# Kernel optimization log

Hardware: AMD Instinct MI355X
Metric: run time of the kernel (lower is better)

Reference implementation:

```python
import jax, jax.numpy as jnp
import numpy as np

N_NODES = 50000
N_EDGES = 400000
D_IN = 2048
D_OUT = 512


def setup_inputs() -> dict:
    key = jax.random.key(0)
    k1, k2, k3 = jax.random.split(key, 3)
    x = jax.random.normal(k1, (N_NODES, D_IN), dtype=jnp.float32)
    edge_index = jax.random.randint(k2, (2, N_EDGES), 0, N_NODES, dtype=jnp.int64)
    # Glorot init like PyG GCNConv
    scale = jnp.sqrt(6.0 / (D_IN + D_OUT)).astype(jnp.float32)
    weight = jax.random.uniform(k3, (D_IN, D_OUT), dtype=jnp.float32, minval=-scale, maxval=scale)
    bias = jnp.zeros((D_OUT,), dtype=jnp.float32)
    return {"x": x, "edge_index": edge_index, "weight": weight, "bias": bias}


def reference(x, edge_index, weight, bias):
    N = x.shape[0]
    # GCNConv(normalize=True): add self-loops, symmetric deg^-1/2 normalization
    loops = jnp.arange(N, dtype=edge_index.dtype)
    src = jnp.concatenate([edge_index[0], loops])  # message sources (x_j)
    dst = jnp.concatenate([edge_index[1], loops])  # aggregation targets
    ones = jnp.ones(dst.shape[0], dtype=x.dtype)
    deg = jax.ops.segment_sum(ones, dst, num_segments=N)  # [N]
    deg_inv_sqrt = jnp.where(deg > 0, jax.lax.rsqrt(deg), 0.0)
    norm = deg_inv_sqrt[src] * deg_inv_sqrt[dst]  # [E+N]
    h = x @ weight  # [N, d_out] linear transform before propagation
    msgs = norm[:, None] * h[src]  # [E+N, d_out]
    out = jax.ops.segment_sum(msgs, dst, num_segments=N) + bias  # [N, d_out]
    return jax.nn.log_softmax(out, axis=1)
```

## Files before the change

kernel.cpp:

```cpp
#include <hip/hip_runtime.h>
#include <stdint.h>

#define D_IN   2048
#define D_OUT  512

typedef __bf16 bf16;
typedef bf16     bf16x8 __attribute__((ext_vector_type(8)));
typedef float    f32x4  __attribute__((ext_vector_type(4)));
typedef uint32_t u32x4  __attribute__((ext_vector_type(4)));

#define GLP(p)  (const __attribute__((address_space(1))) void*)(p)
#define LDSP(p) (__attribute__((address_space(3))) void*)(p)

__global__ void k_count(const int* __restrict__ dstv, int* __restrict__ cnt, int E) {
    int e = blockIdx.x * blockDim.x + threadIdx.x;
    if (e < E) atomicAdd(&cnt[dstv[e]], 1);
}

__global__ void k_dis(const int* __restrict__ cnt, float* __restrict__ dis, int n) {
    int i = blockIdx.x * blockDim.x + threadIdx.x;
    if (i < n) dis[i] = rsqrtf((float)(cnt[i] + 1));
}

__global__ __launch_bounds__(1024) void k_scan1(const int* __restrict__ cnt,
                                                int* __restrict__ offs,
                                                int* __restrict__ bsum, int n) {
    __shared__ int wsum[16], wbase[16];
    const int tid = threadIdx.x, lane = tid & 63, wv = tid >> 6;
    int i = blockIdx.x * 1024 + tid;
    int v = (i < n) ? cnt[i] : 0;
    int x = v;
    #pragma unroll
    for (int d = 1; d < 64; d <<= 1) {
        int y = __shfl_up(x, d);
        if (lane >= d) x += y;
    }
    if (lane == 63) wsum[wv] = x;
    __syncthreads();
    if (tid < 16) {
        int s = 0;
        for (int j = 0; j < tid; ++j) s += wsum[j];
        wbase[tid] = s;
    }
    __syncthreads();
    if (i < n) offs[i] = wbase[wv] + x - v;
    if (tid == 0) bsum[blockIdx.x] = wbase[15] + wsum[15];
}

__global__ void k_scan2(int* __restrict__ bsum, int nb) {
    int t = threadIdx.x;
    if (nb <= 64) {
        int v = (t < nb) ? bsum[t] : 0;
        int x = v;
        #pragma unroll
        for (int d = 1; d < 64; d <<= 1) {
            int y = __shfl_up(x, d);
            if (t >= d) x += y;
        }
        if (t < nb) bsum[t] = x - v;
    } else if (t == 0) {
        int run = 0;
        for (int j = 0; j < nb; ++j) { int v = bsum[j]; bsum[j] = run; run += v; }
    }
}

__global__ void k_scan3(int* __restrict__ offs, const int* __restrict__ bsum, int n) {
    int i = blockIdx.x * blockDim.x + threadIdx.x;
    if (i < n) offs[i] += bsum[i >> 10];
}

__global__ void k_fill(const int* __restrict__ srcv, const int* __restrict__ dstv,
                       const int* __restrict__ offs, int* __restrict__ cur,
                       int* __restrict__ csr, int E) {
    int e = blockIdx.x * blockDim.x + threadIdx.x;
    if (e < E) {
        int d = dstv[e];
        int p = offs[d] + atomicAdd(&cur[d], 1);
        csr[p] = srcv[e];
    }
}

__global__ void k_wt(const float* __restrict__ W, uint16_t* __restrict__ wt) {
    __shared__ float t[32][33];
    int kb = blockIdx.x * 32, nb = blockIdx.y * 32;
    int tx = threadIdx.x, ty = threadIdx.y;
    #pragma unroll
    for (int i = 0; i < 32; i += 8)
        t[ty + i][tx] = W[(size_t)(kb + ty + i) * D_OUT + nb + tx];
    __syncthreads();
    bf16* o = (bf16*)wt;
    #pragma unroll
    for (int i = 0; i < 32; i += 8)
        o[(size_t)(nb + ty + i) * D_IN + kb + tx] = (bf16)t[tx][ty + i];
}

__global__ __launch_bounds__(256) void k_gemm(const float* __restrict__ X,
                                              const uint16_t* __restrict__ WT,
                                              uint16_t* __restrict__ H, int M) {
    __shared__ float    lsA[2][128 * 32];
    __shared__ uint16_t lsB[128 * 64];
    const int nwg = gridDim.x;
    const int b = blockIdx.x;
    const int q = nwg >> 3, r = nwg & 7;
    const int xcd = b & 7, lo = b >> 3;
    const int g = (xcd < r) ? (xcd * (q + 1) + lo) : (r * (q + 1) + (xcd - r) * q + lo);
    const int m0 = (g >> 2) * 128;
    const int n0 = (g & 3) * 128;
    const int tid = threadIdx.x;
    const int w = tid >> 6, lane = tid & 63;
    const int wr = w >> 1, wc = w & 1;
    const int lr = lane & 15, lk = lane >> 4;

    f32x4 acc[4][4];
    #pragma unroll
    for (int m = 0; m < 4; m++)
        #pragma unroll
        for (int n = 0; n < 4; n++) acc[m][n] = (f32x4)(0.0f);

    const float* aSrc[2][4];
    const uint16_t* bSrc[4];
    #pragma unroll
    for (int j = 0; j < 4; j++) {
        int c = w * 4 + j;
        int uidx = c * 64 + lane;
        int row = uidx >> 3, u = uidx & 7;
        int lrow = row;
        if (m0 + row >= M) lrow = (M - 1) - m0;
        const float* rbase = X + (size_t)(m0 + lrow) * D_IN;
        #pragma unroll
        for (int h = 0; h < 2; h++)
            aSrc[h][j] = rbase + h * 32 + (u ^ (row & 7)) * 4;
        bSrc[j] = WT + (size_t)(n0 + row) * D_IN + (u ^ (row & 7)) * 8;
    }

    for (int k0 = 0; k0 < D_IN; k0 += 64) {
        #pragma unroll
        for (int h = 0; h < 2; h++)
            #pragma unroll
            for (int j = 0; j < 4; j++)
                __builtin_amdgcn_global_load_lds(GLP(aSrc[h][j] + k0),
                                                 LDSP(lsA[h] + (w * 4 + j) * 256), 16, 0, 0);
        #pragma unroll
        for (int j = 0; j < 4; j++)
            __builtin_amdgcn_global_load_lds(GLP(bSrc[j] + k0),
                                             LDSP(lsB + (w * 4 + j) * 512), 16, 0, 0);
        __syncthreads();

        #pragma unroll
        for (int kk = 0; kk < 2; kk++) {
            bf16x8 aF[4], bF[4];
            #pragma unroll
            for (int m = 0; m < 4; m++) {
                int row = wr * 64 + m * 16 + lr;
                const float* base = lsA[kk] + row * 32;
                f32x4 a0 = *(const f32x4*)(base + (((2 * lk)    ) ^ (row & 7)) * 4);
                f32x4 a1 = *(const f32x4*)(base + (((2 * lk) + 1) ^ (row & 7)) * 4);
                bf16x8 af;
                af[0] = (bf16)a0[0]; af[1] = (bf16)a0[1]; af[2] = (bf16)a0[2]; af[3] = (bf16)a0[3];
                af[4] = (bf16)a1[0]; af[5] = (bf16)a1[1]; af[6] = (bf16)a1[2]; af[7] = (bf16)a1[3];
                aF[m] = af;
            }
            #pragma unroll
            for (int n = 0; n < 4; n++) {
                int row = wc * 64 + n * 16 + lr;
                bF[n] = *(const bf16x8*)((const bf16*)lsB + row * 64 + (((kk * 4 + lk) ^ (row & 7)) * 8));
            }
            #pragma unroll
            for (int m = 0; m < 4; m++)
                #pragma unroll
                for (int n = 0; n < 4; n++)
                    acc[m][n] = __builtin_amdgcn_mfma_f32_16x16x32_bf16(aF[m], bF[n], acc[m][n], 0, 0, 0);
        }
        __syncthreads();
    }

    #pragma unroll
    for (int m = 0; m < 4; m++) {
        int rbase = m0 + wr * 64 + m * 16 + lk * 4;
        #pragma unroll
        for (int n = 0; n < 4; n++) {
            int col = n0 + wc * 64 + n * 16 + lr;
            #pragma unroll
            for (int j = 0; j < 4; j++) {
                int row = rbase + j;
                if (row < M) {
                    bf16 t = (bf16)acc[m][n][j];
                    H[(size_t)row * D_OUT + col] = __builtin_bit_cast(uint16_t, t);
                }
            }
        }
    }
}

__global__ __launch_bounds__(256) void k_agg(const uint16_t* __restrict__ h,
                                             const int* __restrict__ csr,
                                             const int* __restrict__ offs,
                                             const int* __restrict__ cnt,
                                             const float* __restrict__ dis,
                                             const float* __restrict__ bias,
                                             float* __restrict__ out, int N) {
    const int wv = threadIdx.x >> 6, lane = threadIdx.x & 63;
    const int i = blockIdx.x * 4 + wv;
    if (i >= N) return;
    const float di = dis[i];
    float acc[8];
    {
        u32x4 v = *(const u32x4*)(h + (size_t)i * D_OUT + lane * 8);
        float s2 = di * di;
        #pragma unroll
        for (int k = 0; k < 4; k++) {
            acc[2 * k]     = __builtin_bit_cast(float, v[k] << 16) * s2;
            acc[2 * k + 1] = __builtin_bit_cast(float, v[k] & 0xffff0000u) * s2;
        }
    }
    const int o = offs[i], c = cnt[i];
    for (int e = o; e < o + c; ++e) {
        int s = csr[e];
        float ws = di * dis[s];
        u32x4 v = *(const u32x4*)(h + (size_t)s * D_OUT + lane * 8);
        #pragma unroll
        for (int k = 0; k < 4; k++) {
            acc[2 * k]     += __builtin_bit_cast(float, v[k] << 16) * ws;
            acc[2 * k + 1] += __builtin_bit_cast(float, v[k] & 0xffff0000u) * ws;
        }
    }
    {
        const f32x4* bp = (const f32x4*)(bias + lane * 8);
        f32x4 b0 = bp[0], b1 = bp[1];
        #pragma unroll
        for (int k = 0; k < 4; k++) { acc[k] += b0[k]; acc[4 + k] += b1[k]; }
    }
    float mx = acc[0];
    #pragma unroll
    for (int k = 1; k < 8; k++) mx = fmaxf(mx, acc[k]);
    #pragma unroll
    for (int d = 1; d < 64; d <<= 1) mx = fmaxf(mx, __shfl_xor(mx, d));
    float se = 0.f;
    #pragma unroll
    for (int k = 0; k < 8; k++) se += expf(acc[k] - mx);
    #pragma unroll
    for (int d = 1; d < 64; d <<= 1) se += __shfl_xor(se, d);
    float lse = mx + logf(se);
    f32x4 o0, o1;
    #pragma unroll
    for (int k = 0; k < 4; k++) { o0[k] = acc[k] - lse; o1[k] = acc[4 + k] - lse; }
    f32x4* op = (f32x4*)(out + (size_t)i * D_OUT + lane * 8);
    op[0] = o0; op[1] = o1;
}

extern "C" void kernel_launch(void* const* d_in, const int* in_sizes, int n_in,
                              void* d_out, int out_size, void* d_ws, size_t ws_size,
                              hipStream_t stream) {
    const float* x    = (const float*)d_in[0];
    const int*   ei   = (const int*)d_in[1];
    const float* W    = (const float*)d_in[2];
    const float* bias = (const float*)d_in[3];
    float* out = (float*)d_out;

    const int N = in_sizes[0] / D_IN;
    const int E = in_sizes[1] / 2;
    const int* srcv = ei;
    const int* dstv = ei + E;

    char* p = (char*)d_ws;
    auto carve = [&](size_t b) { void* r = (void*)p; p += (b + 255) & ~(size_t)255; return r; };
    uint16_t* h    = (uint16_t*)carve((size_t)N * D_OUT * 2);
    uint16_t* wt   = (uint16_t*)carve((size_t)D_OUT * D_IN * 2);
    int*      cnt  = (int*)carve((size_t)N * 4);
    int*      cur  = (int*)carve((size_t)N * 4);
    float*    dis  = (float*)carve((size_t)N * 4);
    int*      offs = (int*)carve((size_t)N * 4);
    int*      csr  = (int*)carve((size_t)E * 4);
    int*      bsum = (int*)carve(1024 * 4);

    hipMemsetAsync(cnt, 0, ((size_t)N * 4 + 255 & ~(size_t)255) + (size_t)N * 4, stream);

    k_wt<<<dim3(D_IN / 32, D_OUT / 32), dim3(32, 8), 0, stream>>>(W, wt);
    k_count<<<(E + 255) / 256, 256, 0, stream>>>(dstv, cnt, E);
    k_dis<<<(N + 255) / 256, 256, 0, stream>>>(cnt, dis, N);
    const int nb = (N + 1023) / 1024;
    k_scan1<<<nb, 1024, 0, stream>>>(cnt, offs, bsum, N);
    k_scan2<<<1, 64, 0, stream>>>(bsum, nb);
    k_scan3<<<(N + 255) / 256, 256, 0, stream>>>(offs, bsum, N);
    k_fill<<<(E + 255) / 256, 256, 0, stream>>>(srcv, dstv, offs, cur, csr, E);

    k_gemm<<<((N + 127) / 128) * 4, 256, 0, stream>>>(x, wt, h, N);

    k_agg<<<(N + 3) / 4, 256, 0, stream>>>(h, csr, offs, cnt, dis, bias, out, N);
}
```

Baseline: 342.6 us.

## Fuse small graph-prep kernels and convert GEMM A operand to bf16 at LDS store

Folds the degree-normalization and cursor-reset work into the first scan kernel, and removes the scan-fixup kernel by adding block sums at use sites in fill and aggregate. The memset shrinks accordingly. In the GEMM, the fp32 X tile is now loaded through registers, converted to bf16 once, and stored to a swizzled bf16 LDS tile. This replaces the direct global-to-LDS fp32 copy followed by per-fragment conversion, halving LDS footprint and removing repeated converts. The cost is losing the async global_load_lds path for A, which adds register pressure and load latency inside the loop.

```diff
diff --git a/kernel.cpp b/kernel.cpp
--- a/kernel.cpp
+++ b/kernel.cpp
@@ -17,14 +17,11 @@
     if (e < E) atomicAdd(&cnt[dstv[e]], 1);
 }
 
-__global__ void k_dis(const int* __restrict__ cnt, float* __restrict__ dis, int n) {
-    int i = blockIdx.x * blockDim.x + threadIdx.x;
-    if (i < n) dis[i] = rsqrtf((float)(cnt[i] + 1));
-}
-
 __global__ __launch_bounds__(1024) void k_scan1(const int* __restrict__ cnt,
                                                 int* __restrict__ offs,
-                                                int* __restrict__ bsum, int n) {
+                                                int* __restrict__ bsum,
+                                                float* __restrict__ dis,
+                                                int* __restrict__ cur, int n) {
     __shared__ int wsum[16], wbase[16];
     const int tid = threadIdx.x, lane = tid & 63, wv = tid >> 6;
     int i = blockIdx.x * 1024 + tid;
@@ -43,7 +40,11 @@
         wbase[tid] = s;
     }
     __syncthreads();
-    if (i < n) offs[i] = wbase[wv] + x - v;
+    if (i < n) {
+        offs[i] = wbase[wv] + x - v;
+        dis[i]  = rsqrtf((float)(v + 1));
+        cur[i]  = 0;
+    }
     if (tid == 0) bsum[blockIdx.x] = wbase[15] + wsum[15];
 }
 
@@ -64,18 +65,13 @@
     }
 }
 
-__global__ void k_scan3(int* __restrict__ offs, const int* __restrict__ bsum, int n) {
-    int i = blockIdx.x * blockDim.x + threadIdx.x;
-    if (i < n) offs[i] += bsum[i >> 10];
-}
-
 __global__ void k_fill(const int* __restrict__ srcv, const int* __restrict__ dstv,
-                       const int* __restrict__ offs, int* __restrict__ cur,
-                       int* __restrict__ csr, int E) {
+                       const int* __restrict__ offs, const int* __restrict__ bsum,
+                       int* __restrict__ cur, int* __restrict__ csr, int E) {
     int e = blockIdx.x * blockDim.x + threadIdx.x;
     if (e < E) {
         int d = dstv[e];
-        int p = offs[d] + atomicAdd(&cur[d], 1);
+        int p = offs[d] + bsum[d >> 10] + atomicAdd(&cur[d], 1);
         csr[p] = srcv[e];
     }
 }
@@ -97,7 +93,7 @@
 __global__ __launch_bounds__(256) void k_gemm(const float* __restrict__ X,
                                               const uint16_t* __restrict__ WT,
                                               uint16_t* __restrict__ H, int M) {
-    __shared__ float    lsA[2][128 * 32];
+    __shared__ uint16_t lsA[128 * 64];
     __shared__ uint16_t lsB[128 * 64];
     const int nwg = gridDim.x;
     const int b = blockIdx.x;
@@ -117,33 +113,34 @@
         #pragma unroll
         for (int n = 0; n < 4; n++) acc[m][n] = (f32x4)(0.0f);
 
-    const float* aSrc[2][4];
+    const float* aSrc[4];
+    int aDst[4];
     const uint16_t* bSrc[4];
     #pragma unroll
     for (int j = 0; j < 4; j++) {
-        int c = w * 4 + j;
-        int uidx = c * 64 + lane;
+        int uidx = (w * 4 + j) * 64 + lane;
         int row = uidx >> 3, u = uidx & 7;
         int lrow = row;
         if (m0 + row >= M) lrow = (M - 1) - m0;
-        const float* rbase = X + (size_t)(m0 + lrow) * D_IN;
-        #pragma unroll
-        for (int h = 0; h < 2; h++)
-            aSrc[h][j] = rbase + h * 32 + (u ^ (row & 7)) * 4;
+        aSrc[j] = X + (size_t)(m0 + lrow) * D_IN + u * 8;
+        aDst[j] = row * 64 + (u ^ (row & 7)) * 8;
         bSrc[j] = WT + (size_t)(n0 + row) * D_IN + (u ^ (row & 7)) * 8;
     }
 
     for (int k0 = 0; k0 < D_IN; k0 += 64) {
-        #pragma unroll
-        for (int h = 0; h < 2; h++)
-            #pragma unroll
-            for (int j = 0; j < 4; j++)
-                __builtin_amdgcn_global_load_lds(GLP(aSrc[h][j] + k0),
-                                                 LDSP(lsA[h] + (w * 4 + j) * 256), 16, 0, 0);
         #pragma unroll
         for (int j = 0; j < 4; j++)
             __builtin_amdgcn_global_load_lds(GLP(bSrc[j] + k0),
                                              LDSP(lsB + (w * 4 + j) * 512), 16, 0, 0);
+        #pragma unroll
+        for (int j = 0; j < 4; j++) {
+            f32x4 a0 = *(const f32x4*)(aSrc[j] + k0);
+            f32x4 a1 = *(const f32x4*)(aSrc[j] + k0 + 4);
+            bf16x8 t;
+            t[0] = (bf16)a0[0]; t[1] = (bf16)a0[1]; t[2] = (bf16)a0[2]; t[3] = (bf16)a0[3];
+            t[4] = (bf16)a1[0]; t[5] = (bf16)a1[1]; t[6] = (bf16)a1[2]; t[7] = (bf16)a1[3];
+            *(bf16x8*)(lsA + aDst[j]) = t;
+        }
         __syncthreads();
 
         #pragma unroll
@@ -152,18 +149,12 @@
             #pragma unroll
             for (int m = 0; m < 4; m++) {
                 int row = wr * 64 + m * 16 + lr;
-                const float* base = lsA[kk] + row * 32;
-                f32x4 a0 = *(const f32x4*)(base + (((2 * lk)    ) ^ (row & 7)) * 4);
-                f32x4 a1 = *(const f32x4*)(base + (((2 * lk) + 1) ^ (row & 7)) * 4);
-                bf16x8 af;
-                af[0] = (bf16)a0[0]; af[1] = (bf16)a0[1]; af[2] = (bf16)a0[2]; af[3] = (bf16)a0[3];
-                af[4] = (bf16)a1[0]; af[5] = (bf16)a1[1]; af[6] = (bf16)a1[2]; af[7] = (bf16)a1[3];
-                aF[m] = af;
+                aF[m] = *(const bf16x8*)(lsA + row * 64 + (((kk * 4 + lk) ^ (row & 7)) * 8));
             }
             #pragma unroll
             for (int n = 0; n < 4; n++) {
                 int row = wc * 64 + n * 16 + lr;
-                bF[n] = *(const bf16x8*)((const bf16*)lsB + row * 64 + (((kk * 4 + lk) ^ (row & 7)) * 8));
+                bF[n] = *(const bf16x8*)(lsB + row * 64 + (((kk * 4 + lk) ^ (row & 7)) * 8));
             }
             #pragma unroll
             for (int m = 0; m < 4; m++)
@@ -195,6 +186,7 @@
 __global__ __launch_bounds__(256) void k_agg(const uint16_t* __restrict__ h,
                                              const int* __restrict__ csr,
                                              const int* __restrict__ offs,
+                                             const int* __restrict__ bsum,
                                              const int* __restrict__ cnt,
                                              const float* __restrict__ dis,
                                              const float* __restrict__ bias,
@@ -213,7 +205,7 @@
             acc[2 * k + 1] = __builtin_bit_cast(float, v[k] & 0xffff0000u) * s2;
         }
     }
-    const int o = offs[i], c = cnt[i];
+    const int o = offs[i] + bsum[i >> 10], c = cnt[i];
     for (int e = o; e < o + c; ++e) {
         int s = csr[e];
         float ws = di * dis[s];
@@ -273,18 +265,16 @@
     int*      csr  = (int*)carve((size_t)E * 4);
     int*      bsum = (int*)carve(1024 * 4);
 
-    hipMemsetAsync(cnt, 0, ((size_t)N * 4 + 255 & ~(size_t)255) + (size_t)N * 4, stream);
+    hipMemsetAsync(cnt, 0, (size_t)N * 4, stream);
 
     k_wt<<<dim3(D_IN / 32, D_OUT / 32), dim3(32, 8), 0, stream>>>(W, wt);
     k_count<<<(E + 255) / 256, 256, 0, stream>>>(dstv, cnt, E);
-    k_dis<<<(N + 255) / 256, 256, 0, stream>>>(cnt, dis, N);
     const int nb = (N + 1023) / 1024;
-    k_scan1<<<nb, 1024, 0, stream>>>(cnt, offs, bsum, N);
+    k_scan1<<<nb, 1024, 0, stream>>>(cnt, offs, bsum, dis, cur, N);
     k_scan2<<<1, 64, 0, stream>>>(bsum, nb);
-    k_scan3<<<(N + 255) / 256, 256, 0, stream>>>(offs, bsum, N);
-    k_fill<<<(E + 255) / 256, 256, 0, stream>>>(srcv, dstv, offs, cur, csr, E);
+    k_fill<<<(E + 255) / 256, 256, 0, stream>>>(srcv, dstv, offs, bsum, cur, csr, E);
 
     k_gemm<<<((N + 127) / 128) * 4, 256, 0, stream>>>(x, wt, h, N);
 
-    k_agg<<<(N + 3) / 4, 256, 0, stream>>>(h, csr, offs, cnt, dis, bias, out, N);
-}
+    k_agg<<<(N + 3) / 4, 256, 0, stream>>>(h, csr, offs, bsum, cnt, dis, bias, out, N);
+}
```

After: 369.1 us. +7.7%, slower.
